# Performance work log

Measured on AMD Instinct MI355X. Metric: run time of the kernel, lower is better.

## Reference

```python
import jax, jax.numpy as jnp
import numpy as np

N, IN_DIM, L, K, D = 131072, 128, 16, 8, 50
ENC_H, DEC_H, HEAD_H, DF = 64, 16, 64, 1.0


def setup_inputs() -> dict:
    key = jax.random.key(0)
    ks = jax.random.split(key, 20)
    s = lambda k, shape, fan: jax.random.normal(k, shape, jnp.float32) * (1.0 / np.sqrt(fan))
    return {
        "x": jax.random.normal(ks[0], (N, IN_DIM), jnp.float32),
        # encoder: in -> 64 -> 64 -> L
        "We1": s(ks[1], (IN_DIM, ENC_H), IN_DIM), "be1": jnp.zeros((ENC_H,), jnp.float32),
        "We2": s(ks[2], (ENC_H, ENC_H), ENC_H),   "be2": jnp.zeros((ENC_H,), jnp.float32),
        "We3": s(ks[3], (ENC_H, L), ENC_H),       "be3": jnp.zeros((L,), jnp.float32),
        # decoder: L -> 16 -> in
        "Wd1": s(ks[4], (L, DEC_H), L),           "bd1": jnp.zeros((DEC_H,), jnp.float32),
        "Wd2": s(ks[5], (DEC_H, IN_DIM), DEC_H),  "bd2": jnp.zeros((IN_DIM,), jnp.float32),
        # K per-cluster survival heads: (L+in) -> 64 -> num_durations
        "Wh1": s(ks[6], (K, L + IN_DIM, HEAD_H), L + IN_DIM), "bh1": jnp.zeros((K, HEAD_H), jnp.float32),
        "Wh2": s(ks[7], (K, HEAD_H, D), HEAD_H),              "bh2": jnp.zeros((K, D), jnp.float32),
        # cluster centers buffer
        "centers": jax.random.normal(ks[8], (K, L), jnp.float32) * 0.05,
    }


def _student_t_sim(z, centers, df):
    # z: [N, L], centers: [K, L] -> q: [N, K]
    dist2 = jnp.sum((z[:, None, :] - centers[None, :, :]) ** 2, axis=-1)
    logits = -0.5 * (df + 1.0) * jnp.log1p(dist2 / df)
    return jax.nn.softmax(logits, axis=1)


def reference(x, We1, be1, We2, be2, We3, be3, Wd1, bd1, Wd2, bd2,
              Wh1, bh1, Wh2, bh2, centers):
    relu = jax.nn.relu
    # encoder (eval mode: dropout off, non-variational)
    e = relu(x @ We1 + be1)
    e = relu(e @ We2 + be2)
    z = e @ We3 + be3                      # [N, L]
    q = _student_t_sim(z, centers, DF)     # [N, K]
    h = jnp.concatenate([z, x], axis=1)    # [N, L+in]
    # cluster-argmax routing to per-cluster heads: compute all K, select winner
    cluster_idx = jnp.argmax(q, axis=1)    # [N]
    h1 = relu(jnp.einsum("nf,kfh->nkh", h, Wh1) + bh1[None])   # [N, K, H]
    lg = jnp.einsum("nkh,khd->nkd", h1, Wh2) + bh2[None]       # [N, K, D]
    surv_logits = jnp.take_along_axis(lg, cluster_idx[:, None, None], axis=1)[:, 0]  # [N, D]
    # decoder + reconstruction loss per sample
    d = relu(z @ Wd1 + bd1)
    x_hat = d @ Wd2 + bd2                  # [N, in]
    rec_ps = jnp.mean((x_hat - x) ** 2, axis=1)
    kld = jnp.zeros((x.shape[0],), x.dtype)
    return z, q, surv_logits, x_hat, rec_ps, kld
```

## Files before the change

kernel.cpp:

```cpp
#include <hip/hip_runtime.h>

#define NS 131072
#define KC 8
typedef unsigned long long u64;

#define LD4(P) (*reinterpret_cast<const float4*>(&sm[(P)]))
#define ST4(P) (*reinterpret_cast<float4*>(&sm[(P)]))
#define GL4(P) (*reinterpret_cast<const float4*>(&(P)))

#define FMA4(ACCR, AV, B) do { \
  ACCR[0]=fmaf((AV),(B).x,ACCR[0]); ACCR[1]=fmaf((AV),(B).y,ACCR[1]); \
  ACCR[2]=fmaf((AV),(B).z,ACCR[2]); ACCR[3]=fmaf((AV),(B).w,ACCR[3]); } while(0)

#define K4(ACC, ABASE, ASTR, AK, BBASE, BSTR, JOFF, BK) do { \
  const float4 b0=LD4((BBASE)+((BK)*4+0)*(BSTR)+(JOFF)); \
  const float4 b1=LD4((BBASE)+((BK)*4+1)*(BSTR)+(JOFF)); \
  const float4 b2=LD4((BBASE)+((BK)*4+2)*(BSTR)+(JOFF)); \
  const float4 b3=LD4((BBASE)+((BK)*4+3)*(BSTR)+(JOFF)); \
  _Pragma("unroll") \
  for (int m_ = 0; m_ < 8; ++m_) { \
    const float4 av = LD4((ABASE)+(st+8*m_)*(ASTR)+(AK)*4); \
    FMA4(ACC[m_], av.x, b0); FMA4(ACC[m_], av.y, b1); \
    FMA4(ACC[m_], av.z, b2); FMA4(ACC[m_], av.w, b3); } \
} while(0)

#define INIT84(ACC, BPTR, OFF) do { \
  const float4 u_ = *reinterpret_cast<const float4*>(&(BPTR)[(OFF)]); \
  _Pragma("unroll") for (int m_=0;m_<8;++m_){ \
    ACC[m_][0]=u_.x; ACC[m_][1]=u_.y; ACC[m_][2]=u_.z; ACC[m_][3]=u_.w; } } while(0)

#define RELU84(ACC) do { _Pragma("unroll") for (int m_=0;m_<8;++m_) \
  { _Pragma("unroll") for (int j_=0;j_<4;++j_) ACC[m_][j_]=fmaxf(ACC[m_][j_],0.f); } } while(0)

#define WRITE_E(ACC) do { _Pragma("unroll") for (int m_=0;m_<8;++m_){ \
  ST4(EA + (st+8*m_)*68 + job) = \
    make_float4(ACC[m_][0],ACC[m_][1],ACC[m_][2],ACC[m_][3]); } } while(0)

#define STAGE_X() do { \
  ST4(AR + xr0*20 + xcc)     = rx0; \
  ST4(AR + xr0*20 + xcc + 4) = rx1; } while(0)
#define STAGE_W() do { \
  ST4(WB + wr*68 + wcc)     = rw0; \
  ST4(WB + wr*68 + wcc + 4) = rw1; } while(0)

#define AR   0
#define EA   1280
#define WB   5632
#define WD1i 6720
#define SMW  6976

__global__ __launch_bounds__(128, 2) void k_enc(
    const float* __restrict__ x,
    const float* __restrict__ We1, const float* __restrict__ be1,
    const float* __restrict__ We2, const float* __restrict__ be2,
    const float* __restrict__ We3, const float* __restrict__ be3,
    const float* __restrict__ Wd1, const float* __restrict__ bd1,
    const float* __restrict__ Wd2, const float* __restrict__ bd2,
    const float* __restrict__ centers,
    float* __restrict__ out_z, float* __restrict__ out_q,
    float* __restrict__ xhat, float* __restrict__ rec, float* __restrict__ kld,
    int* __restrict__ cidx, int* __restrict__ counts)
{
    __shared__ float sm[SMW];
    const int t  = threadIdx.x;
    const int ot = t & 15, st = t >> 4;
    const int job = ot * 4;
    const int s0 = blockIdx.x * 64;
    const int xr0 = t >> 1, xcc = (t & 1) * 8;
    const int wr  = t >> 3, wcc = (t & 7) * 8;

    {
        float acc1[8][4];
        INIT84(acc1, be1, job);
        float4 rx0 = GL4(x[(size_t)(s0+xr0)*128 + xcc]);
        float4 rx1 = GL4(x[(size_t)(s0+xr0)*128 + xcc + 4]);
        float4 rw0 = GL4(We1[(size_t)wr*64 + wcc]);
        float4 rw1 = GL4(We1[(size_t)wr*64 + wcc + 4]);
        #pragma unroll 1
        for (int c = 0; c < 8; ++c) {
            __syncthreads();
            STAGE_X(); STAGE_W();
            __syncthreads();
            if (c < 7) {
                rx0 = GL4(x[(size_t)(s0+xr0)*128 + (c+1)*16 + xcc]);
                rx1 = GL4(x[(size_t)(s0+xr0)*128 + (c+1)*16 + xcc + 4]);
                rw0 = GL4(We1[(size_t)((c+1)*16 + wr)*64 + wcc]);
                rw1 = GL4(We1[(size_t)((c+1)*16 + wr)*64 + wcc + 4]);
            }
            #pragma unroll
            for (int kc = 0; kc < 4; ++kc) K4(acc1, AR, 20, kc, WB, 68, job, kc);
        }
        __syncthreads();
        RELU84(acc1);
        WRITE_E(acc1);
    }

    {
        float acc2[8][4];
        INIT84(acc2, be2, job);
        float4 rw0 = GL4(We2[(size_t)wr*64 + wcc]);
        float4 rw1 = GL4(We2[(size_t)wr*64 + wcc + 4]);
        #pragma unroll 1
        for (int c = 0; c < 4; ++c) {
            __syncthreads();
            STAGE_W();
            __syncthreads();
            if (c < 3) {
                rw0 = GL4(We2[(size_t)((c+1)*16 + wr)*64 + wcc]);
                rw1 = GL4(We2[(size_t)((c+1)*16 + wr)*64 + wcc + 4]);
            }
            #pragma unroll
            for (int kc = 0; kc < 4; ++kc) K4(acc2, EA, 68, c*4 + kc, WB, 68, job, kc);
        }
        __syncthreads();
        RELU84(acc2);
        WRITE_E(acc2);
        {   const int r3 = t >> 2, c3 = (t & 3) * 4;
            ST4(WB + r3*16 + c3)        = GL4(We3[(size_t)r3*16 + c3]);
            ST4(WB + (r3+32)*16 + c3)   = GL4(We3[(size_t)(r3+32)*16 + c3]); }
        if (t < 64) ST4(WD1i + (t >> 2)*16 + (t & 3)*4) =
            GL4(Wd1[(t >> 2)*16 + (t & 3)*4]);
    }
    __syncthreads();

    float zac[8];
    {   const float b3v = be3[ot];
        #pragma unroll
        for (int m = 0; m < 8; ++m) zac[m] = b3v; }
    #pragma unroll 2
    for (int kc = 0; kc < 16; ++kc) {
        const float w0 = sm[WB + (kc*4+0)*16 + ot];
        const float w1 = sm[WB + (kc*4+1)*16 + ot];
        const float w2 = sm[WB + (kc*4+2)*16 + ot];
        const float w3 = sm[WB + (kc*4+3)*16 + ot];
        #pragma unroll
        for (int m = 0; m < 8; ++m) {
            const float4 av = LD4(EA + (st + 8*m)*68 + kc*4);
            float s = zac[m];
            s = fmaf(av.x, w0, s); s = fmaf(av.y, w1, s);
            s = fmaf(av.z, w2, s); s = fmaf(av.w, w3, s);
            zac[m] = s;
        }
    }
    #pragma unroll
    for (int m = 0; m < 8; ++m)
        out_z[(size_t)(s0 + st + 8*m)*16 + ot] = zac[m];
    __syncthreads();
    #pragma unroll
    for (int m = 0; m < 8; ++m) sm[AR + (st + 8*m)*20 + ot] = zac[m];
    {
        ST4(WB + wr*68 + wcc)     = GL4(Wd2[(size_t)wr*128 + wcc]);
        ST4(WB + wr*68 + wcc + 4) = GL4(Wd2[(size_t)wr*128 + wcc + 4]); }
    __syncthreads();

    if (t < 64) {
        const float4 z0 = LD4(AR + t*20 + 0), z1 = LD4(AR + t*20 + 4);
        const float4 z2 = LD4(AR + t*20 + 8), z3 = LD4(AR + t*20 + 12);
        const float zz[16] = {z0.x,z0.y,z0.z,z0.w, z1.x,z1.y,z1.z,z1.w,
                              z2.x,z2.y,z2.z,z2.w, z3.x,z3.y,z3.z,z3.w};
        float d2[KC];
        #pragma unroll
        for (int k = 0; k < KC; ++k) {
            float acc = 0.f;
            #pragma unroll
            for (int l = 0; l < 16; ++l) {
                const float dl = zz[l] - centers[k*16 + l];
                acc = fmaf(dl, dl, acc);
            }
            d2[k] = acc;
        }
        float lgt[KC], ex[KC];
        float mm = -1e30f;
        #pragma unroll
        for (int k = 0; k < KC; ++k) { lgt[k] = -log1pf(d2[k]); mm = fmaxf(mm, lgt[k]); }
        float ssum = 0.f;
        #pragma unroll
        for (int k = 0; k < KC; ++k) { ex[k] = expf(lgt[k] - mm); ssum += ex[k]; }
        const float inv = 1.f / ssum;
        float4* oq = reinterpret_cast<float4*>(&out_q[(size_t)(s0 + t)*8]);
        oq[0] = make_float4(ex[0]*inv, ex[1]*inv, ex[2]*inv, ex[3]*inv);
        oq[1] = make_float4(ex[4]*inv, ex[5]*inv, ex[6]*inv, ex[7]*inv);
        int ci = 0; float best = d2[0];
        #pragma unroll
        for (int k = 1; k < KC; ++k) if (d2[k] < best) { best = d2[k]; ci = k; }
        cidx[s0 + t] = ci;
        #pragma unroll
        for (int k = 0; k < KC; ++k) {
            const u64 mk = __ballot(ci == k);
            if (t == 0 && mk) atomicAdd(&counts[k], (int)__popcll(mk));
        }
        kld[s0 + t] = 0.f;
    }

    {
        float w[16];
        #pragma unroll
        for (int k = 0; k < 16; ++k) w[k] = sm[WD1i + k*16 + ot];
        const float bb = bd1[ot];
        float dac[8];
        #pragma unroll
        for (int m = 0; m < 8; ++m) {
            const int r = st + 8*m;
            float s = bb;
            #pragma unroll
            for (int kc = 0; kc < 4; ++kc) {
                const float4 av = LD4(AR + r*20 + kc*4);
                s = fmaf(av.x, w[kc*4+0], s); s = fmaf(av.y, w[kc*4+1], s);
                s = fmaf(av.z, w[kc*4+2], s); s = fmaf(av.w, w[kc*4+3], s);
            }
            dac[m] = fmaxf(s, 0.f);
        }
        __syncthreads();
        #pragma unroll
        for (int m = 0; m < 8; ++m) sm[AR + (st + 8*m)*20 + ot] = dac[m];
    }
    __syncthreads();

    float rp[8] = {0.f,0.f,0.f,0.f,0.f,0.f,0.f,0.f};
    float4 rw20 = GL4(Wd2[(size_t)wr*128 + 64 + wcc]);
    float4 rw21 = GL4(Wd2[(size_t)wr*128 + 64 + wcc + 4]);
    {
        float accx[8][4];
        INIT84(accx, bd2, job);
        #pragma unroll
        for (int kc = 0; kc < 4; ++kc) K4(accx, AR, 20, kc, WB, 68, job, kc);
        #pragma unroll
        for (int m = 0; m < 8; ++m) {
            const int r = st + 8*m;
            const float4 xa = GL4(x[(size_t)(s0+r)*128 + job]);
            float df;
            df=accx[m][0]-xa.x; rp[m]=fmaf(df,df,rp[m]);
            df=accx[m][1]-xa.y; rp[m]=fmaf(df,df,rp[m]);
            df=accx[m][2]-xa.z; rp[m]=fmaf(df,df,rp[m]);
            df=accx[m][3]-xa.w; rp[m]=fmaf(df,df,rp[m]);
            *reinterpret_cast<float4*>(&xhat[(size_t)(s0+r)*128 + job]) =
                make_float4(accx[m][0],accx[m][1],accx[m][2],accx[m][3]);
        }
    }
    __syncthreads();
    ST4(WB + wr*68 + wcc)     = rw20;
    ST4(WB + wr*68 + wcc + 4) = rw21;
    __syncthreads();
    {
        float accx[8][4];
        INIT84(accx, bd2, 64 + job);
        #pragma unroll
        for (int kc = 0; kc < 4; ++kc) K4(accx, AR, 20, kc, WB, 68, job, kc);
        #pragma unroll
        for (int m = 0; m < 8; ++m) {
            const int r = st + 8*m;
            const float4 xa = GL4(x[(size_t)(s0+r)*128 + 64 + job]);
            float df;
            df=accx[m][0]-xa.x; rp[m]=fmaf(df,df,rp[m]);
            df=accx[m][1]-xa.y; rp[m]=fmaf(df,df,rp[m]);
            df=accx[m][2]-xa.z; rp[m]=fmaf(df,df,rp[m]);
            df=accx[m][3]-xa.w; rp[m]=fmaf(df,df,rp[m]);
            *reinterpret_cast<float4*>(&xhat[(size_t)(s0+r)*128 + 64 + job]) =
                make_float4(accx[m][0],accx[m][1],accx[m][2],accx[m][3]);
        }
    }
    #pragma unroll
    for (int m = 0; m < 8; ++m) {
        float v = rp[m];
        v += __shfl_xor(v, 1); v += __shfl_xor(v, 2);
        v += __shfl_xor(v, 4); v += __shfl_xor(v, 8);
        if (ot == 0) rec[s0 + st + 8*m] = v * (1.f/128.f);
    }
}

__global__ void k_scan(const int* __restrict__ counts,
                       int* __restrict__ bases, int* __restrict__ cursors)
{
    if (threadIdx.x == 0) {
        int acc = 0;
        for (int k = 0; k < KC; ++k) { bases[k] = acc; cursors[k] = acc; acc += counts[k]; }
    }
}

__global__ __launch_bounds__(256) void k_scatter(
    const int* __restrict__ cidx, int* __restrict__ cursors, int* __restrict__ seg)
{
    const int s = blockIdx.x * 256 + threadIdx.x;
    const int lane = threadIdx.x & 63;
    const int ci = cidx[s];
    #pragma unroll
    for (int k = 0; k < KC; ++k) {
        const u64 mk = __ballot(ci == k);
        if (ci == k) {
            const int leader = __ffsll(mk) - 1;
            int base = 0;
            if (lane == leader) base = atomicAdd(&cursors[k], (int)__popcll(mk));
            base = __shfl(base, leader, 64);
            seg[base + (int)__popcll(mk & (((u64)1 << lane) - 1))] = s;
        }
    }
}

__global__ __launch_bounds__(128, 2) void k_heads(
    const float* __restrict__ x, const float* __restrict__ zread,
    const float* __restrict__ Wh1, const float* __restrict__ bh1,
    const float* __restrict__ Wh2, const float* __restrict__ bh2,
    const int* __restrict__ counts, const int* __restrict__ bases,
    const int* __restrict__ seg,
    float* __restrict__ surv)
{
    __shared__ float sm[SMW];
    __shared__ int idxs[64];
    const int t  = threadIdx.x;
    const int ot = t & 15, st = t >> 4;
    const int job = ot * 4;
    const int xr0 = t >> 1, xcc = (t & 1) * 8;
    const int wr  = t >> 3, wcc = (t & 7) * 8;

    int kk = -1, chunk = 0, pref = 0;
    #pragma unroll
    for (int q = 0; q < KC; ++q) {
        const int ck = (counts[q] + 63) >> 6;
        if (kk < 0) {
            if ((int)blockIdx.x < pref + ck) { kk = q; chunk = (int)blockIdx.x - pref; }
            pref += ck;
        }
    }
    if (kk < 0) return;
    kk    = __builtin_amdgcn_readfirstlane(kk);
    chunk = __builtin_amdgcn_readfirstlane(chunk);
    const int cnt  = __builtin_amdgcn_readfirstlane(counts[kk]);
    const int base = __builtin_amdgcn_readfirstlane(bases[kk]);

    if (t < 64) {
        const int i = chunk*64 + t;
        idxs[t] = seg[base + ((i < cnt) ? i : (cnt - 1))];
    }
    __syncthreads();
    const int irow = idxs[xr0];

    {
        float acc1[8][4];
        INIT84(acc1, bh1, (size_t)kk*64 + job);
        {
            ST4(AR + xr0*20 + xcc)     = GL4(zread[(size_t)irow*16 + xcc]);
            ST4(AR + xr0*20 + xcc + 4) = GL4(zread[(size_t)irow*16 + xcc + 4]);
            ST4(WB + wr*68 + wcc)     = GL4(Wh1[((size_t)kk*144 + wr)*64 + wcc]);
            ST4(WB + wr*68 + wcc + 4) = GL4(Wh1[((size_t)kk*144 + wr)*64 + wcc + 4]); }
        __syncthreads();
        float4 rx0 = GL4(x[(size_t)irow*128 + xcc]);
        float4 rx1 = GL4(x[(size_t)irow*128 + xcc + 4]);
        float4 rw0 = GL4(Wh1[((size_t)kk*144 + 16 + wr)*64 + wcc]);
        float4 rw1 = GL4(Wh1[((size_t)kk*144 + 16 + wr)*64 + wcc + 4]);
        #pragma unroll
        for (int kc = 0; kc < 4; ++kc) K4(acc1, AR, 20, kc, WB, 68, job, kc);
        #pragma unroll 1
        for (int c = 0; c < 8; ++c) {
            __syncthreads();
            STAGE_X(); STAGE_W();
            __syncthreads();
            if (c < 7) {
                rx0 = GL4(x[(size_t)irow*128 + (c+1)*16 + xcc]);
                rx1 = GL4(x[(size_t)irow*128 + (c+1)*16 + xcc + 4]);
                rw0 = GL4(Wh1[((size_t)kk*144 + 16 + (c+1)*16 + wr)*64 + wcc]);
                rw1 = GL4(Wh1[((size_t)kk*144 + 16 + (c+1)*16 + wr)*64 + wcc + 4]);
            }
            #pragma unroll
            for (int kc = 0; kc < 4; ++kc) K4(acc1, AR, 20, kc, WB, 68, job, kc);
        }
        __syncthreads();
        RELU84(acc1);
        WRITE_E(acc1);
    }

    float acc2[8][4];
    {   float4 bz;
        bz.x = (job+0 < 50) ? bh2[(size_t)kk*50 + job+0] : 0.f;
        bz.y = (job+1 < 50) ? bh2[(size_t)kk*50 + job+1] : 0.f;
        bz.z = (job+2 < 50) ? bh2[(size_t)kk*50 + job+2] : 0.f;
        bz.w = (job+3 < 50) ? bh2[(size_t)kk*50 + job+3] : 0.f;
        #pragma unroll
        for (int m = 0; m < 8; ++m) {
            acc2[m][0] = bz.x; acc2[m][1] = bz.y;
            acc2[m][2] = bz.z; acc2[m][3] = bz.w;
        } }
    float4 rv0, rv1;
    {   const size_t wrow = ((size_t)kk*64 + wr)*50;
        rv0.x = (wcc+0 < 50) ? Wh2[wrow + wcc+0] : 0.f;
        rv0.y = (wcc+1 < 50) ? Wh2[wrow + wcc+1] : 0.f;
        rv0.z = (wcc+2 < 50) ? Wh2[wrow + wcc+2] : 0.f;
        rv0.w = (wcc+3 < 50) ? Wh2[wrow + wcc+3] : 0.f;
        rv1.x = (wcc+4 < 50) ? Wh2[wrow + wcc+4] : 0.f;
        rv1.y = (wcc+5 < 50) ? Wh2[wrow + wcc+5] : 0.f;
        rv1.z = (wcc+6 < 50) ? Wh2[wrow + wcc+6] : 0.f;
        rv1.w = (wcc+7 < 50) ? Wh2[wrow + wcc+7] : 0.f; }
    #pragma unroll 1
    for (int c = 0; c < 4; ++c) {
        __syncthreads();
        ST4(WB + wr*68 + wcc)     = rv0;
        ST4(WB + wr*68 + wcc + 4) = rv1;
        __syncthreads();
        if (c < 3) {
            const size_t wrow = ((size_t)kk*64 + (c+1)*16 + wr)*50;
            rv0.x = (wcc+0 < 50) ? Wh2[wrow + wcc+0] : 0.f;
            rv0.y = (wcc+1 < 50) ? Wh2[wrow + wcc+1] : 0.f;
            rv0.z = (wcc+2 < 50) ? Wh2[wrow + wcc+2] : 0.f;
            rv0.w = (wcc+3 < 50) ? Wh2[wrow + wcc+3] : 0.f;
            rv1.x = (wcc+4 < 50) ? Wh2[wrow + wcc+4] : 0.f;
            rv1.y = (wcc+5 < 50) ? Wh2[wrow + wcc+5] : 0.f;
            rv1.z = (wcc+6 < 50) ? Wh2[wrow + wcc+6] : 0.f;
            rv1.w = (wcc+7 < 50) ? Wh2[wrow + wcc+7] : 0.f;
        }
        #pragma unroll
        for (int kc = 0; kc < 4; ++kc) K4(acc2, EA, 68, c*4 + kc, WB, 68, job, kc);
    }

    #pragma unroll
    for (int m = 0; m < 8; ++m) {
        const int r = st + 8*m;
        if (chunk*64 + r < cnt) {
            float* so = &surv[(size_t)idxs[r]*50 + job];
            if (ot < 12) {
                *reinterpret_cast<float2*>(&so[0]) = make_float2(acc2[m][0], acc2[m][1]);
                *reinterpret_cast<float2*>(&so[2]) = make_float2(acc2[m][2], acc2[m][3]);
            } else if (ot == 12) {
                *reinterpret_cast<float2*>(&so[0]) = make_float2(acc2[m][0], acc2[m][1]);
            }
        }
    }
}

extern "C" void kernel_launch(void* const* d_in, const int* in_sizes, int n_in,
                              void* d_out, int out_size, void* d_ws, size_t ws_size,
                              hipStream_t stream)
{
    const float* x   = (const float*)d_in[0];
    const float* We1 = (const float*)d_in[1];
    const float* be1 = (const float*)d_in[2];
    const float* We2 = (const float*)d_in[3];
    const float* be2 = (const float*)d_in[4];
    const float* We3 = (const float*)d_in[5];
    const float* be3 = (const float*)d_in[6];
    const float* Wd1 = (const float*)d_in[7];
    const float* bd1 = (const float*)d_in[8];
    const float* Wd2 = (const float*)d_in[9];
    const float* bd2 = (const float*)d_in[10];
    const float* Wh1 = (const float*)d_in[11];
    const float* bh1 = (const float*)d_in[12];
    const float* Wh2 = (const float*)d_in[13];
    const float* bh2 = (const float*)d_in[14];
    const float* cen = (const float*)d_in[15];
    float* out = (float*)d_out;

    float* out_z  = out;
    float* out_q  = out + (size_t)NS * 16;
    float* out_sv = out + (size_t)NS * 24;
    float* out_xh = out + (size_t)NS * 74;
    float* out_rc = out + (size_t)NS * 202;
    float* out_kl = out + (size_t)NS * 203;

    int* cidx    = (int*)d_ws;
    int* counts  = cidx + NS;
    int* bases   = counts + KC;
    int* cursors = bases + KC;
    int* seg     = cursors + KC;

    hipMemsetAsync(counts, 0, KC * sizeof(int), stream);

    k_enc<<<dim3(NS / 64), dim3(128), 0, stream>>>(
        x, We1, be1, We2, be2, We3, be3, Wd1, bd1, Wd2, bd2, cen,
        out_z, out_q, out_xh, out_rc, out_kl, cidx, counts);

    k_scan<<<dim3(1), dim3(64), 0, stream>>>(counts, bases, cursors);

    k_scatter<<<dim3(NS / 256), dim3(256), 0, stream>>>(cidx, cursors, seg);

    k_heads<<<dim3(NS / 64 + KC), dim3(128), 0, stream>>>(
        x, out_z, Wh1, bh1, Wh2, bh2, counts, bases, seg, out_sv);
}
```

Before: 448.1 us.

## Double-buffer shared-memory tiles to halve barriers in encoder and head GEMM loops

Splits the shared X and W staging areas into ping-pong buffers so the next chunk is written to shared memory while the current one is consumed, leaving one barrier per iteration instead of two. The shared layout is reorganised (Wd2 preloaded into both halves, z/decoder scratch aliased over the E area) so the decoder's two halves run in one loop without restaging Wd2. Shared memory per block grows from about 27KB to about 36KB, which could cut occupancy, and the aliasing of ZD with EA relies on barrier ordering being correct.

```diff
diff --git a/kernel.cpp b/kernel.cpp
--- a/kernel.cpp
+++ b/kernel.cpp
@@ -36,18 +36,20 @@
   ST4(EA + (st+8*m_)*68 + job) = \
     make_float4(ACC[m_][0],ACC[m_][1],ACC[m_][2],ACC[m_][3]); } } while(0)
 
-#define STAGE_X() do { \
-  ST4(AR + xr0*20 + xcc)     = rx0; \
-  ST4(AR + xr0*20 + xcc + 4) = rx1; } while(0)
-#define STAGE_W() do { \
-  ST4(WB + wr*68 + wcc)     = rw0; \
-  ST4(WB + wr*68 + wcc + 4) = rw1; } while(0)
-
-#define AR   0
-#define EA   1280
-#define WB   5632
-#define WD1i 6720
-#define SMW  6976
+#define STAGE_XB(B) do { \
+  ST4((B) + xr0*20 + xcc)     = rx0; \
+  ST4((B) + xr0*20 + xcc + 4) = rx1; } while(0)
+#define STAGE_WB(B) do { \
+  ST4((B) + wr*68 + wcc)     = rw0; \
+  ST4((B) + wr*68 + wcc + 4) = rw1; } while(0)
+
+#define XA   0
+#define XB   1280
+#define WA   2560
+#define WB_  3648
+#define EA   4736
+#define ZD   4736
+#define SMW  9088
 
 __global__ __launch_bounds__(128, 2) void k_enc(
     const float* __restrict__ x,
@@ -76,21 +78,27 @@
         float4 rx1 = GL4(x[(size_t)(s0+xr0)*128 + xcc + 4]);
         float4 rw0 = GL4(We1[(size_t)wr*64 + wcc]);
         float4 rw1 = GL4(We1[(size_t)wr*64 + wcc + 4]);
+        STAGE_XB(XA); STAGE_WB(WA);
+        rx0 = GL4(x[(size_t)(s0+xr0)*128 + 16 + xcc]);
+        rx1 = GL4(x[(size_t)(s0+xr0)*128 + 16 + xcc + 4]);
+        rw0 = GL4(We1[(size_t)(16 + wr)*64 + wcc]);
+        rw1 = GL4(We1[(size_t)(16 + wr)*64 + wcc + 4]);
+        __syncthreads();
         #pragma unroll 1
         for (int c = 0; c < 8; ++c) {
+            const int XC = (c & 1) ? XB : XA, WC = (c & 1) ? WB_ : WA;
+            const int XN = (c & 1) ? XA : XB, WN = (c & 1) ? WA : WB_;
+            if (c < 7) { STAGE_XB(XN); STAGE_WB(WN); }
+            if (c < 6) {
+                rx0 = GL4(x[(size_t)(s0+xr0)*128 + (c+2)*16 + xcc]);
+                rx1 = GL4(x[(size_t)(s0+xr0)*128 + (c+2)*16 + xcc + 4]);
+                rw0 = GL4(We1[(size_t)((c+2)*16 + wr)*64 + wcc]);
+                rw1 = GL4(We1[(size_t)((c+2)*16 + wr)*64 + wcc + 4]);
+            }
+            #pragma unroll
+            for (int kc = 0; kc < 4; ++kc) K4(acc1, XC, 20, kc, WC, 68, job, kc);
             __syncthreads();
-            STAGE_X(); STAGE_W();
-            __syncthreads();
-            if (c < 7) {
-                rx0 = GL4(x[(size_t)(s0+xr0)*128 + (c+1)*16 + xcc]);
-                rx1 = GL4(x[(size_t)(s0+xr0)*128 + (c+1)*16 + xcc + 4]);
-                rw0 = GL4(We1[(size_t)((c+1)*16 + wr)*64 + wcc]);
-                rw1 = GL4(We1[(size_t)((c+1)*16 + wr)*64 + wcc + 4]);
-            }
-            #pragma unroll
-            for (int kc = 0; kc < 4; ++kc) K4(acc1, AR, 20, kc, WB, 68, job, kc);
-        }
-        __syncthreads();
+        }
         RELU84(acc1);
         WRITE_E(acc1);
     }
@@ -100,27 +108,36 @@
         INIT84(acc2, be2, job);
         float4 rw0 = GL4(We2[(size_t)wr*64 + wcc]);
         float4 rw1 = GL4(We2[(size_t)wr*64 + wcc + 4]);
+        STAGE_WB(WA);
+        rw0 = GL4(We2[(size_t)(16 + wr)*64 + wcc]);
+        rw1 = GL4(We2[(size_t)(16 + wr)*64 + wcc + 4]);
+        __syncthreads();
         #pragma unroll 1
         for (int c = 0; c < 4; ++c) {
+            const int WC = (c & 1) ? WB_ : WA;
+            const int WN = (c & 1) ? WA : WB_;
+            if (c < 3) STAGE_WB(WN);
+            if (c < 2) {
+                rw0 = GL4(We2[(size_t)((c+2)*16 + wr)*64 + wcc]);
+                rw1 = GL4(We2[(size_t)((c+2)*16 + wr)*64 + wcc + 4]);
+            }
+            #pragma unroll
+            for (int kc = 0; kc < 4; ++kc) K4(acc2, EA, 68, c*4 + kc, WC, 68, job, kc);
             __syncthreads();
-            STAGE_W();
-            __syncthreads();
-            if (c < 3) {
-                rw0 = GL4(We2[(size_t)((c+1)*16 + wr)*64 + wcc]);
-                rw1 = GL4(We2[(size_t)((c+1)*16 + wr)*64 + wcc + 4]);
-            }
-            #pragma unroll
-            for (int kc = 0; kc < 4; ++kc) K4(acc2, EA, 68, c*4 + kc, WB, 68, job, kc);
-        }
-        __syncthreads();
+        }
         RELU84(acc2);
         WRITE_E(acc2);
-        {   const int r3 = t >> 2, c3 = (t & 3) * 4;
-            ST4(WB + r3*16 + c3)        = GL4(We3[(size_t)r3*16 + c3]);
-            ST4(WB + (r3+32)*16 + c3)   = GL4(We3[(size_t)(r3+32)*16 + c3]); }
-        if (t < 64) ST4(WD1i + (t >> 2)*16 + (t & 3)*4) =
-            GL4(Wd1[(t >> 2)*16 + (t & 3)*4]);
-    }
+    }
+
+    {   const int r3 = t >> 2, c3 = (t & 3) * 4;
+        ST4(XA + r3*16 + c3)      = GL4(We3[(size_t)r3*16 + c3]);
+        ST4(XA + (r3+32)*16 + c3) = GL4(We3[(size_t)(r3+32)*16 + c3]); }
+    if (t < 64) ST4(XB + (t >> 2)*16 + (t & 3)*4) =
+        GL4(Wd1[(t >> 2)*16 + (t & 3)*4]);
+    ST4(WA  + wr*68 + wcc)     = GL4(Wd2[(size_t)wr*128 + wcc]);
+    ST4(WA  + wr*68 + wcc + 4) = GL4(Wd2[(size_t)wr*128 + wcc + 4]);
+    ST4(WB_ + wr*68 + wcc)     = GL4(Wd2[(size_t)wr*128 + 64 + wcc]);
+    ST4(WB_ + wr*68 + wcc + 4) = GL4(Wd2[(size_t)wr*128 + 64 + wcc + 4]);
     __syncthreads();
 
     float zac[8];
@@ -129,10 +146,10 @@
         for (int m = 0; m < 8; ++m) zac[m] = b3v; }
     #pragma unroll 2
     for (int kc = 0; kc < 16; ++kc) {
-        const float w0 = sm[WB + (kc*4+0)*16 + ot];
-        const float w1 = sm[WB + (kc*4+1)*16 + ot];
-        const float w2 = sm[WB + (kc*4+2)*16 + ot];
-        const float w3 = sm[WB + (kc*4+3)*16 + ot];
+        const float w0 = sm[XA + (kc*4+0)*16 + ot];
+        const float w1 = sm[XA + (kc*4+1)*16 + ot];
+        const float w2 = sm[XA + (kc*4+2)*16 + ot];
+        const float w3 = sm[XA + (kc*4+3)*16 + ot];
         #pragma unroll
         for (int m = 0; m < 8; ++m) {
             const float4 av = LD4(EA + (st + 8*m)*68 + kc*4);
@@ -147,15 +164,12 @@
         out_z[(size_t)(s0 + st + 8*m)*16 + ot] = zac[m];
     __syncthreads();
     #pragma unroll
-    for (int m = 0; m < 8; ++m) sm[AR + (st + 8*m)*20 + ot] = zac[m];
-    {
-        ST4(WB + wr*68 + wcc)     = GL4(Wd2[(size_t)wr*128 + wcc]);
-        ST4(WB + wr*68 + wcc + 4) = GL4(Wd2[(size_t)wr*128 + wcc + 4]); }
+    for (int m = 0; m < 8; ++m) sm[ZD + (st + 8*m)*20 + ot] = zac[m];
     __syncthreads();
 
     if (t < 64) {
-        const float4 z0 = LD4(AR + t*20 + 0), z1 = LD4(AR + t*20 + 4);
-        const float4 z2 = LD4(AR + t*20 + 8), z3 = LD4(AR + t*20 + 12);
+        const float4 z0 = LD4(ZD + t*20 + 0), z1 = LD4(ZD + t*20 + 4);
+        const float4 z2 = LD4(ZD + t*20 + 8), z3 = LD4(ZD + t*20 + 12);
         const float zz[16] = {z0.x,z0.y,z0.z,z0.w, z1.x,z1.y,z1.z,z1.w,
                               z2.x,z2.y,z2.z,z2.w, z3.x,z3.y,z3.z,z3.w};
         float d2[KC];
@@ -195,7 +209,7 @@
     {
         float w[16];
         #pragma unroll
-        for (int k = 0; k < 16; ++k) w[k] = sm[WD1i + k*16 + ot];
+        for (int k = 0; k < 16; ++k) w[k] = sm[XB + k*16 + ot];
         const float bb = bd1[ot];
         float dac[8];
         #pragma unroll
@@ -204,7 +218,7 @@
             float s = bb;
             #pragma unroll
             for (int kc = 0; kc < 4; ++kc) {
-                const float4 av = LD4(AR + r*20 + kc*4);
+                const float4 av = LD4(ZD + r*20 + kc*4);
                 s = fmaf(av.x, w[kc*4+0], s); s = fmaf(av.y, w[kc*4+1], s);
                 s = fmaf(av.z, w[kc*4+2], s); s = fmaf(av.w, w[kc*4+3], s);
             }
@@ -212,50 +226,27 @@
         }
         __syncthreads();
         #pragma unroll
-        for (int m = 0; m < 8; ++m) sm[AR + (st + 8*m)*20 + ot] = dac[m];
-    }
-    __syncthreads();
+        for (int m = 0; m < 8; ++m) sm[ZD + (st + 8*m)*20 + ot] = dac[m];
+    }
 
     float rp[8] = {0.f,0.f,0.f,0.f,0.f,0.f,0.f,0.f};
-    float4 rw20 = GL4(Wd2[(size_t)wr*128 + 64 + wcc]);
-    float4 rw21 = GL4(Wd2[(size_t)wr*128 + 64 + wcc + 4]);
-    {
+    #pragma unroll
+    for (int h = 0; h < 2; ++h) {
+        const int WH = h ? WB_ : WA;
         float accx[8][4];
-        INIT84(accx, bd2, job);
-        #pragma unroll
-        for (int kc = 0; kc < 4; ++kc) K4(accx, AR, 20, kc, WB, 68, job, kc);
+        INIT84(accx, bd2, h*64 + job);
+        #pragma unroll
+        for (int kc = 0; kc < 4; ++kc) K4(accx, ZD, 20, kc, WH, 68, job, kc);
         #pragma unroll
         for (int m = 0; m < 8; ++m) {
             const int r = st + 8*m;
-            const float4 xa = GL4(x[(size_t)(s0+r)*128 + job]);
+            const float4 xa = GL4(x[(size_t)(s0+r)*128 + h*64 + job]);
             float df;
             df=accx[m][0]-xa.x; rp[m]=fmaf(df,df,rp[m]);
             df=accx[m][1]-xa.y; rp[m]=fmaf(df,df,rp[m]);
             df=accx[m][2]-xa.z; rp[m]=fmaf(df,df,rp[m]);
             df=accx[m][3]-xa.w; rp[m]=fmaf(df,df,rp[m]);
-            *reinterpret_cast<float4*>(&xhat[(size_t)(s0+r)*128 + job]) =
-                make_float4(accx[m][0],accx[m][1],accx[m][2],accx[m][3]);
-        }
-    }
-    __syncthreads();
-    ST4(WB + wr*68 + wcc)     = rw20;
-    ST4(WB + wr*68 + wcc + 4) = rw21;
-    __syncthreads();
-    {
-        float accx[8][4];
-        INIT84(accx, bd2, 64 + job);
-        #pragma unroll
-        for (int kc = 0; kc < 4; ++kc) K4(accx, AR, 20, kc, WB, 68, job, kc);
-        #pragma unroll
-        for (int m = 0; m < 8; ++m) {
-            const int r = st + 8*m;
-            const float4 xa = GL4(x[(size_t)(s0+r)*128 + 64 + job]);
-            float df;
-            df=accx[m][0]-xa.x; rp[m]=fmaf(df,df,rp[m]);
-            df=accx[m][1]-xa.y; rp[m]=fmaf(df,df,rp[m]);
-            df=accx[m][2]-xa.z; rp[m]=fmaf(df,df,rp[m]);
-            df=accx[m][3]-xa.w; rp[m]=fmaf(df,df,rp[m]);
-            *reinterpret_cast<float4*>(&xhat[(size_t)(s0+r)*128 + 64 + job]) =
+            *reinterpret_cast<float4*>(&xhat[(size_t)(s0+r)*128 + h*64 + job]) =
                 make_float4(accx[m][0],accx[m][1],accx[m][2],accx[m][3]);
         }
     }
@@ -337,23 +328,20 @@
     {
         float acc1[8][4];
         INIT84(acc1, bh1, (size_t)kk*64 + job);
-        {
-            ST4(AR + xr0*20 + xcc)     = GL4(zread[(size_t)irow*16 + xcc]);
-            ST4(AR + xr0*20 + xcc + 4) = GL4(zread[(size_t)irow*16 + xcc + 4]);
-            ST4(WB + wr*68 + wcc)     = GL4(Wh1[((size_t)kk*144 + wr)*64 + wcc]);
-            ST4(WB + wr*68 + wcc + 4) = GL4(Wh1[((size_t)kk*144 + wr)*64 + wcc + 4]); }
-        __syncthreads();
+        ST4(XA + xr0*20 + xcc)     = GL4(zread[(size_t)irow*16 + xcc]);
+        ST4(XA + xr0*20 + xcc + 4) = GL4(zread[(size_t)irow*16 + xcc + 4]);
+        ST4(WA + wr*68 + wcc)      = GL4(Wh1[((size_t)kk*144 + wr)*64 + wcc]);
+        ST4(WA + wr*68 + wcc + 4)  = GL4(Wh1[((size_t)kk*144 + wr)*64 + wcc + 4]);
         float4 rx0 = GL4(x[(size_t)irow*128 + xcc]);
         float4 rx1 = GL4(x[(size_t)irow*128 + xcc + 4]);
         float4 rw0 = GL4(Wh1[((size_t)kk*144 + 16 + wr)*64 + wcc]);
         float4 rw1 = GL4(Wh1[((size_t)kk*144 + 16 + wr)*64 + wcc + 4]);
-        #pragma unroll
-        for (int kc = 0; kc < 4; ++kc) K4(acc1, AR, 20, kc, WB, 68, job, kc);
+        __syncthreads();
         #pragma unroll 1
-        for (int c = 0; c < 8; ++c) {
-            __syncthreads();
-            STAGE_X(); STAGE_W();
-            __syncthreads();
+        for (int c = 0; c < 9; ++c) {
+            const int XC = (c & 1) ? XB : XA, WC = (c & 1) ? WB_ : WA;
+            const int XN = (c & 1) ? XA : XB, WN = (c & 1) ? WA : WB_;
+            if (c < 8) { STAGE_XB(XN); STAGE_WB(WN); }
             if (c < 7) {
                 rx0 = GL4(x[(size_t)irow*128 + (c+1)*16 + xcc]);
                 rx1 = GL4(x[(size_t)irow*128 + (c+1)*16 + xcc + 4]);
@@ -361,54 +349,51 @@
                 rw1 = GL4(Wh1[((size_t)kk*144 + 16 + (c+1)*16 + wr)*64 + wcc + 4]);
             }
             #pragma unroll
-            for (int kc = 0; kc < 4; ++kc) K4(acc1, AR, 20, kc, WB, 68, job, kc);
-        }
-        __syncthreads();
+            for (int kc = 0; kc < 4; ++kc) K4(acc1, XC, 20, kc, WC, 68, job, kc);
+            __syncthreads();
+        }
         RELU84(acc1);
         WRITE_E(acc1);
     }
 
     float acc2[8][4];
-    {   float4 bz;
-        bz.x = (job+0 < 50) ? bh2[(size_t)kk*50 + job+0] : 0.f;
-        bz.y = (job+1 < 50) ? bh2[(size_t)kk*50 + job+1] : 0.f;
-        bz.z = (job+2 < 50) ? bh2[(size_t)kk*50 + job+2] : 0.f;
-        bz.w = (job+3 < 50) ? bh2[(size_t)kk*50 + job+3] : 0.f;
+    {
         #pragma unroll
         for (int m = 0; m < 8; ++m) {
-            acc2[m][0] = bz.x; acc2[m][1] = bz.y;
-            acc2[m][2] = bz.z; acc2[m][3] = bz.w;
-        } }
-    float4 rv0, rv1;
-    {   const size_t wrow = ((size_t)kk*64 + wr)*50;
-        rv0.x = (wcc+0 < 50) ? Wh2[wrow + wcc+0] : 0.f;
-        rv0.y = (wcc+1 < 50) ? Wh2[wrow + wcc+1] : 0.f;
-        rv0.z = (wcc+2 < 50) ? Wh2[wrow + wcc+2] : 0.f;
-        rv0.w = (wcc+3 < 50) ? Wh2[wrow + wcc+3] : 0.f;
-        rv1.x = (wcc+4 < 50) ? Wh2[wrow + wcc+4] : 0.f;
-        rv1.y = (wcc+5 < 50) ? Wh2[wrow + wcc+5] : 0.f;
-        rv1.z = (wcc+6 < 50) ? Wh2[wrow + wcc+6] : 0.f;
-        rv1.w = (wcc+7 < 50) ? Wh2[wrow + wcc+7] : 0.f; }
-    #pragma unroll 1
-    for (int c = 0; c < 4; ++c) {
+            acc2[m][0] = (job+0 < 50) ? bh2[(size_t)kk*50 + job+0] : 0.f;
+            acc2[m][1] = (job+1 < 50) ? bh2[(size_t)kk*50 + job+1] : 0.f;
+            acc2[m][2] = (job+2 < 50) ? bh2[(size_t)kk*50 + job+2] : 0.f;
+            acc2[m][3] = (job+3 < 50) ? bh2[(size_t)kk*50 + job+3] : 0.f;
+        }
+    }
+    #define LDWH2(RV0, RV1, CROW) do { \
+        const size_t wrow_ = ((size_t)kk*64 + (CROW) + wr)*50; \
+        RV0.x = (wcc+0 < 50) ? Wh2[wrow_ + wcc+0] : 0.f; \
+        RV0.y = (wcc+1 < 50) ? Wh2[wrow_ + wcc+1] : 0.f; \
+        RV0.z = (wcc+2 < 50) ? Wh2[wrow_ + wcc+2] : 0.f; \
+        RV0.w = (wcc+3 < 50) ? Wh2[wrow_ + wcc+3] : 0.f; \
+        RV1.x = (wcc+4 < 50) ? Wh2[wrow_ + wcc+4] : 0.f; \
+        RV1.y = (wcc+5 < 50) ? Wh2[wrow_ + wcc+5] : 0.f; \
+        RV1.z = (wcc+6 < 50) ? Wh2[wrow_ + wcc+6] : 0.f; \
+        RV1.w = (wcc+7 < 50) ? Wh2[wrow_ + wcc+7] : 0.f; } while(0)
+    {
+        float4 rw0, rw1;
+        LDWH2(rw0, rw1, 0);
+        STAGE_WB(WA);
+        LDWH2(rw0, rw1, 16);
         __syncthreads();
-        ST4(WB + wr*68 + wcc)     = rv0;
-        ST4(WB + wr*68 + wcc + 4) = rv1;
-        __syncthreads();
-        if (c < 3) {
-            const size_t wrow = ((size_t)kk*64 + (c+1)*16 + wr)*50;
-            rv0.x = (wcc+0 < 50) ? Wh2[wrow + wcc+0] : 0.f;
-            rv0.y = (wcc+1 < 50) ? Wh2[wrow + wcc+1] : 0.f;
-            rv0.z = (wcc+2 < 50) ? Wh2[wrow + wcc+2] : 0.f;
-            rv0.w = (wcc+3 < 50) ? Wh2[wrow + wcc+3] : 0.f;
-            rv1.x = (wcc+4 < 50) ? Wh2[wrow + wcc+4] : 0.f;
-            rv1.y = (wcc+5 < 50) ? Wh2[wrow + wcc+5] : 0.f;
-            rv1.z = (wcc+6 < 50) ? Wh2[wrow + wcc+6] : 0.f;
-            rv1.w = (wcc+7 < 50) ? Wh2[wrow + wcc+7] : 0.f;
-        }
-        #pragma unroll
-        for (int kc = 0; kc < 4; ++kc) K4(acc2, EA, 68, c*4 + kc, WB, 68, job, kc);
-    }
+        #pragma unroll 1
+        for (int c = 0; c < 4; ++c) {
+            const int WC = (c & 1) ? WB_ : WA;
+            const int WN = (c & 1) ? WA : WB_;
+            if (c < 3) STAGE_WB(WN);
+            if (c < 2) LDWH2(rw0, rw1, (c+2)*16);
+            #pragma unroll
+            for (int kc = 0; kc < 4; ++kc) K4(acc2, EA, 68, c*4 + kc, WC, 68, job, kc);
+            __syncthreads();
+        }
+    }
+    #undef LDWH2
 
     #pragma unroll
     for (int m = 0; m < 8; ++m) {
```

Measured after the change: 458.6 us. +2.3%, slower.
